# Optimization experiments

Measured on AMD Instinct MI355X. Metric: run time of the kernel, lower is better.

The kernel has to match this reference:

```python
import jax, jax.numpy as jnp
import numpy as np

WS = 7        # window_size
SHIFT = 3     # shift_size
HEADS = 6
DIM = 192
HIDDEN = DIM * 6  # mlp_ratio=6
EPS = 1e-5


def _rel_pos_index(ws):
    # static relative-position index, (ws*ws, ws*ws) int
    coords = np.stack(np.meshgrid(np.arange(ws), np.arange(ws), indexing='ij')).reshape(2, -1)
    rel = coords[:, :, None] - coords[:, None, :]            # (2, N, N)
    rel = rel.transpose(1, 2, 0)                             # (N, N, 2)
    rel[:, :, 0] += ws - 1
    rel[:, :, 1] += ws - 1
    rel[:, :, 0] *= 2 * ws - 1
    return rel.sum(-1)


def _layernorm(t, g, b):
    m = t.mean(-1, keepdims=True)
    v = jnp.mean((t - m) ** 2, axis=-1, keepdims=True)
    return (t - m) * jax.lax.rsqrt(v + EPS) * g + b


def setup_inputs() -> dict:
    key = jax.random.key(0)
    ks = jax.random.split(key, 8)
    B, H, W = 16, 56, 56
    x = jax.random.normal(ks[0], (B, H * W, DIM), dtype=jnp.float32)
    p = lambda k, s: (jax.random.normal(k, s, dtype=jnp.float32) * 0.02)
    return {
        'x': x, 'H': H, 'W': W,
        'ln1_g': jnp.ones((DIM,), jnp.float32), 'ln1_b': jnp.zeros((DIM,), jnp.float32),
        'qkv_w': p(ks[1], (3 * DIM, DIM)), 'qkv_b': jnp.zeros((3 * DIM,), jnp.float32),
        'rpb': p(ks[2], ((2 * WS - 1) ** 2, HEADS)),
        'proj_w': p(ks[3], (DIM, DIM)), 'proj_b': jnp.zeros((DIM,), jnp.float32),
        'ln2_g': jnp.ones((DIM,), jnp.float32), 'ln2_b': jnp.zeros((DIM,), jnp.float32),
        'fc1_w': p(ks[4], (HIDDEN, DIM)), 'fc1_b': jnp.zeros((HIDDEN,), jnp.float32),
        'fc2_w': p(ks[5], (DIM, HIDDEN)), 'fc2_b': jnp.zeros((DIM,), jnp.float32),
    }


def reference(x, H, W, ln1_g, ln1_b, qkv_w, qkv_b, rpb, proj_w, proj_b,
              ln2_g, ln2_b, fc1_w, fc1_b, fc2_w, fc2_b):
    B, L, C = x.shape
    hd = C // HEADS
    shortcut = x
    h = _layernorm(x, ln1_g, ln1_b).reshape(B, H, W, C)
    pad_r = (WS - W % WS) % WS
    pad_b = (WS - H % WS) % WS
    h = jnp.pad(h, ((0, 0), (0, pad_b), (0, pad_r), (0, 0)))
    Hp, Wp = H + pad_b, W + pad_r
    if SHIFT > 0:
        h = jnp.roll(h, (-SHIFT, -SHIFT), axis=(1, 2))
    # window partition -> (nW*B, WS*WS, C)
    h = h.reshape(B, Hp // WS, WS, Wp // WS, WS, C).transpose(0, 1, 3, 2, 4, 5)
    h = h.reshape(-1, WS * WS, C)
    nB, N, _ = h.shape
    qkv = (h @ qkv_w.T + qkv_b).reshape(nB, N, 3, HEADS, hd).transpose(2, 0, 3, 1, 4)
    q, k, v = qkv[0], qkv[1], qkv[2]       # (nB, heads, N, hd)
    scale = hd ** -0.5
    attn = jnp.einsum('bhnd,bhmd->bhnm', q * scale, k)
    idx = _rel_pos_index(WS)
    bias = rpb[idx.reshape(-1)].reshape(N, N, HEADS).transpose(2, 0, 1)  # (heads, N, N)
    attn = jax.nn.softmax(attn + bias[None], axis=-1)
    out = jnp.einsum('bhnm,bhmd->bhnd', attn, v).transpose(0, 2, 1, 3).reshape(nB, N, C)
    out = out @ proj_w.T + proj_b
    # window reverse -> (B, Hp, Wp, C)
    out = out.reshape(B, Hp // WS, Wp // WS, WS, WS, C).transpose(0, 1, 3, 2, 4, 5)
    out = out.reshape(B, Hp, Wp, C)
    if SHIFT > 0:
        out = jnp.roll(out, (SHIFT, SHIFT), axis=(1, 2))
    out = out[:, :H, :W, :].reshape(B, H * W, C)
    x = shortcut + out
    h2 = _layernorm(x, ln2_g, ln2_b)
    h2 = jax.nn.gelu(h2 @ fc1_w.T + fc1_b, approximate=False)
    return x + (h2 @ fc2_w.T + fc2_b)
```

## Files before the change

kernel.cpp:

```cpp
#include <hip/hip_runtime.h>

typedef unsigned short u16;
typedef __bf16 bf16x8 __attribute__((ext_vector_type(8)));
typedef float f32x4 __attribute__((ext_vector_type(4)));

#define AS1 __attribute__((address_space(1)))
#define AS3 __attribute__((address_space(3)))

__device__ __forceinline__ void gld16(const void* g, void* l) {
  __builtin_amdgcn_global_load_lds((const AS1 void*)g, (AS3 void*)l, 16, 0, 0);
}

__device__ __forceinline__ u16 f2bf(float f) {
  union { float f; unsigned int u; } v; v.f = f;
  unsigned int u = v.u;
  u += 0x7fffu + ((u >> 16) & 1u);
  return (u16)(u >> 16);
}
__device__ __forceinline__ float bf2f(u16 h) {
  union { unsigned int u; float f; } v; v.u = ((unsigned int)h) << 16; return v.f;
}
__device__ __forceinline__ float gelu_f(float v) {
  float u = v * (1.5957691216f + 0.0713548163f * v * v);
  return v * __frcp_rn(1.0f + __expf(-u));
}

__global__ __launch_bounds__(256) void cast_weights(
    const float* __restrict__ w0, const float* __restrict__ w1,
    const float* __restrict__ w2, const float* __restrict__ w3,
    u16* __restrict__ o0, u16* __restrict__ o1,
    u16* __restrict__ o2, u16* __restrict__ o3) {
  int i = blockIdx.x * 256 + threadIdx.x;
  if (i < 110592) o0[i] = f2bf(w0[i]);
  if (i < 36864)  o1[i] = f2bf(w1[i]);
  if (i < 221184) o2[i] = f2bf(w2[i]);
  if (i < 221184) o3[i] = f2bf(w3[i]);
}

__global__ __launch_bounds__(256) void build_btab(
    const float* __restrict__ rpb, float* __restrict__ btab) {
  int id = blockIdx.x * 256 + threadIdx.x;
  int head = id >> 12;
  int m = (id >> 6) & 63;
  int r = id & 63;
  float v;
  if (m >= 49) v = -1e30f;
  else if (r >= 49) v = 0.0f;
  else {
    int mi = m / 7, mj = m - mi * 7;
    int ri = r / 7, rj = r - ri * 7;
    v = rpb[((ri - mi + 6) * 13 + (rj - mj + 6)) * 6 + head];
  }
  btab[id] = v;
}

__global__ __launch_bounds__(256) void ln_kernel(
    const float* __restrict__ x, const float* __restrict__ g,
    const float* __restrict__ b, u16* __restrict__ out) {
  int row = blockIdx.x * 4 + (threadIdx.x >> 6);
  int lane = threadIdx.x & 63;
  const float* xr = x + (long)row * 192;
  float e0 = xr[lane], e1 = xr[lane + 64], e2 = xr[lane + 128];
  float s = e0 + e1 + e2;
  #pragma unroll
  for (int o = 1; o < 64; o <<= 1) s += __shfl_xor(s, o);
  float mean = s * (1.0f / 192.0f);
  float d0 = e0 - mean, d1 = e1 - mean, d2 = e2 - mean;
  float q = d0 * d0 + d1 * d1 + d2 * d2;
  #pragma unroll
  for (int o = 1; o < 64; o <<= 1) q += __shfl_xor(q, o);
  float rstd = rsqrtf(q * (1.0f / 192.0f) + 1e-5f);
  u16* orow = out + (long)row * 192;
  orow[lane]       = f2bf(d0 * rstd * g[lane]       + b[lane]);
  orow[lane + 64]  = f2bf(d1 * rstd * g[lane + 64]  + b[lane + 64]);
  orow[lane + 128] = f2bf(d2 * rstd * g[lane + 128] + b[lane + 128]);
}

template<int MODE>
__global__ __launch_bounds__(256, 4) void gemm_kernel(
    const u16* __restrict__ A, const u16* __restrict__ W,
    const float* __restrict__ bias, const float* __restrict__ resid,
    void* __restrict__ out, int N, int K) {
  __shared__ u16 lds[18432];
  float* ct = (float*)lds;
  int tid = threadIdx.x;
  int wave = tid >> 6, lane = tid & 63;
  int wm = wave >> 1, wn = wave & 1;
  int quad = lane >> 4, l15 = lane & 15;
  long bm = (long)blockIdx.x * 128;
  int bn = blockIdx.y * 64;

  f32x4 acc[4][2] = {};
  for (int kc = 0; kc < K; kc += 96) {
    if (kc > 0) __syncthreads();
    int t0 = wave * 9;
    #pragma unroll
    for (int ti = 0; ti < 9; ti++) {
      int t = t0 + ti;
      int isB = t >= 24;
      int tt = isB ? t - 24 : t;
      int grp = tt / 3, kt = tt - grp * 3;
      const u16* g = isB
          ? (W + (long)(bn + grp * 16 + l15) * K + kc + kt * 32 + quad * 8)
          : (A + (bm + grp * 16 + l15) * K + kc + kt * 32 + quad * 8);
      gld16(g, &lds[(isB ? 12288 : 0) + tt * 512]);
    }
    __syncthreads();
    #pragma unroll
    for (int kt = 0; kt < 3; kt++) {
      bf16x8 af[4], bfr[2];
      #pragma unroll
      for (int mt = 0; mt < 4; mt++)
        af[mt] = *(const bf16x8*)&lds[((wm * 4 + mt) * 3 + kt) * 512 + lane * 8];
      #pragma unroll
      for (int nt = 0; nt < 2; nt++)
        bfr[nt] = *(const bf16x8*)&lds[12288 + ((wn * 2 + nt) * 3 + kt) * 512 + lane * 8];
      #pragma unroll
      for (int mt = 0; mt < 4; mt++)
        #pragma unroll
        for (int nt = 0; nt < 2; nt++)
          acc[mt][nt] = __builtin_amdgcn_mfma_f32_16x16x32_bf16(af[mt], bfr[nt], acc[mt][nt], 0, 0, 0);
    }
  }
  __syncthreads();
  #pragma unroll
  for (int nt = 0; nt < 2; nt++) {
    int col = wn * 32 + nt * 16 + l15;
    float bi = bias[bn + col];
    #pragma unroll
    for (int mt = 0; mt < 4; mt++) {
      int row0 = wm * 64 + mt * 16 + quad * 4;
      #pragma unroll
      for (int j = 0; j < 4; j++)
        ct[(row0 + j) * 66 + col] = acc[mt][nt][j] + bi;
    }
  }
  __syncthreads();
  #pragma unroll
  for (int it = 0; it < 8; it++) {
    int c = it * 256 + tid;
    int row = c >> 4, cg = (c & 15) * 4;
    float4 v = *(const float4*)&ct[row * 66 + cg];
    long idx = (bm + row) * (long)N + bn + cg;
    if (MODE == 2) {
      const float4 rv = *(const float4*)(resid + idx);
      v.x += rv.x; v.y += rv.y; v.z += rv.z; v.w += rv.w;
      *(float4*)((float*)out + idx) = v;
    } else {
      if (MODE == 1) {
        v.x = gelu_f(v.x); v.y = gelu_f(v.y); v.z = gelu_f(v.z); v.w = gelu_f(v.w);
      }
      uint2 pk;
      pk.x = (unsigned int)f2bf(v.x) | ((unsigned int)f2bf(v.y) << 16);
      pk.y = (unsigned int)f2bf(v.z) | ((unsigned int)f2bf(v.w) << 16);
      *(uint2*)((u16*)out + idx) = pk;
    }
  }
}

__global__ __launch_bounds__(256) void attn_kernel(
    const u16* __restrict__ qkv, const float* __restrict__ btab,
    u16* __restrict__ attn) {
  __shared__ u16 lds[4 * 7552];
  int tid = threadIdx.x;
  int wave = tid >> 6, lane = tid & 63;
  int quad = lane >> 4, l15 = lane & 15;
  int w = blockIdx.x * 4 + wave;
  int win = w / 6, head = w - win * 6;
  int b = win >> 6, wy = (win >> 3) & 7, wx = win & 7;
  u16* lq = lds + wave * 7552;
  u16* lk = lq + 2560;
  u16* lvt = lq + 5120;
  float* rsum = (float*)(lq + 7424);
  u16* lp = lq;

  #pragma unroll
  for (int p = 0; p < 4; p++) {
    int n = p * 16 + (lane >> 2);
    int qtr = (lane & 3) * 8;
    uint4 qv = {}, kv = {}, vv = {};
    if (n < 49) {
      int i = n / 7, j = n - i * 7;
      int y = wy * 7 + i + 3;  if (y >= 56) y -= 56;
      int xx = wx * 7 + j + 3; if (xx >= 56) xx -= 56;
      long base = ((long)(b * 3136 + y * 56 + xx)) * 576 + head * 32 + qtr;
      qv = *(const uint4*)(qkv + base);
      kv = *(const uint4*)(qkv + base + 192);
      vv = *(const uint4*)(qkv + base + 384);
    }
    *(uint4*)&lq[n * 40 + qtr] = qv;
    *(uint4*)&lk[n * 40 + qtr] = kv;
    const u16* vp = (const u16*)&vv;
    #pragma unroll
    for (int d = 0; d < 8; d++) lvt[(qtr + d) * 72 + n] = vp[d];
  }
  __syncthreads();

  bf16x8 ka[4], qb[4];
  #pragma unroll
  for (int t = 0; t < 4; t++) {
    ka[t] = *(const bf16x8*)&lk[(t * 16 + l15) * 40 + quad * 8];
    qb[t] = *(const bf16x8*)&lq[(t * 16 + l15) * 40 + quad * 8];
  }
  f32x4 s[4][4];
  const f32x4 fz = {0.0f, 0.0f, 0.0f, 0.0f};
  #pragma unroll
  for (int tm = 0; tm < 4; tm++)
    #pragma unroll
    for (int tr = 0; tr < 4; tr++)
      s[tm][tr] = __builtin_amdgcn_mfma_f32_16x16x32_bf16(ka[tm], qb[tr], fz, 0, 0, 0);

  const float scale = 0.17677669529663687f;
  const float* bt = btab + head * 4096;
  float mx[4] = {-1e30f, -1e30f, -1e30f, -1e30f};
  #pragma unroll
  for (int tm = 0; tm < 4; tm++) {
    int m0 = tm * 16 + quad * 4;
    #pragma unroll
    for (int tr = 0; tr < 4; tr++) {
      int r = tr * 16 + l15;
      #pragma unroll
      for (int j = 0; j < 4; j++) {
        float v = s[tm][tr][j] * scale + bt[(m0 + j) * 64 + r];
        s[tm][tr][j] = v;
        mx[tr] = fmaxf(mx[tr], v);
      }
    }
  }
  #pragma unroll
  for (int tr = 0; tr < 4; tr++) {
    mx[tr] = fmaxf(mx[tr], __shfl_xor(mx[tr], 16));
    mx[tr] = fmaxf(mx[tr], __shfl_xor(mx[tr], 32));
  }
  float sm[4] = {0.f, 0.f, 0.f, 0.f};
  #pragma unroll
  for (int tm = 0; tm < 4; tm++) {
    #pragma unroll
    for (int tr = 0; tr < 4; tr++) {
      int r = tr * 16 + l15;
      float e0 = __expf(s[tm][tr][0] - mx[tr]);
      float e1 = __expf(s[tm][tr][1] - mx[tr]);
      float e2 = __expf(s[tm][tr][2] - mx[tr]);
      float e3 = __expf(s[tm][tr][3] - mx[tr]);
      sm[tr] += (e0 + e1) + (e2 + e3);
      uint2 pk;
      pk.x = (unsigned int)f2bf(e0) | ((unsigned int)f2bf(e1) << 16);
      pk.y = (unsigned int)f2bf(e2) | ((unsigned int)f2bf(e3) << 16);
      *(uint2*)&lp[r * 72 + tm * 16 + quad * 4] = pk;
    }
  }
  #pragma unroll
  for (int tr = 0; tr < 4; tr++) {
    sm[tr] += __shfl_xor(sm[tr], 16);
    sm[tr] += __shfl_xor(sm[tr], 32);
  }
  if (quad == 0) {
    #pragma unroll
    for (int tr = 0; tr < 4; tr++) rsum[tr * 16 + l15] = 1.0f / sm[tr];
  }
  __syncthreads();

  f32x4 o[4][2] = {};
  #pragma unroll
  for (int ks = 0; ks < 2; ks++) {
    bf16x8 vb0 = *(const bf16x8*)&lvt[(l15) * 72 + ks * 32 + quad * 8];
    bf16x8 vb1 = *(const bf16x8*)&lvt[(16 + l15) * 72 + ks * 32 + quad * 8];
    #pragma unroll
    for (int rt = 0; rt < 4; rt++) {
      bf16x8 pf = *(const bf16x8*)&lp[(rt * 16 + l15) * 72 + ks * 32 + quad * 8];
      o[rt][0] = __builtin_amdgcn_mfma_f32_16x16x32_bf16(pf, vb0, o[rt][0], 0, 0, 0);
      o[rt][1] = __builtin_amdgcn_mfma_f32_16x16x32_bf16(pf, vb1, o[rt][1], 0, 0, 0);
    }
  }
  #pragma unroll
  for (int rt = 0; rt < 4; rt++) {
    #pragma unroll
    for (int j = 0; j < 4; j++) {
      int r = rt * 16 + quad * 4 + j;
      if (r < 49) {
        float inv = rsum[r];
        int i = r / 7, jj = r - i * 7;
        int y = wy * 7 + i + 3;   if (y >= 56) y -= 56;
        int xx = wx * 7 + jj + 3; if (xx >= 56) xx -= 56;
        long base = ((long)(b * 3136 + y * 56 + xx)) * 192 + head * 32 + l15;
        attn[base]      = f2bf(o[rt][0][j] * inv);
        attn[base + 16] = f2bf(o[rt][1][j] * inv);
      }
    }
  }
}

extern "C" void kernel_launch(void* const* d_in, const int* in_sizes, int n_in,
                              void* d_out, int out_size, void* d_ws, size_t ws_size,
                              hipStream_t stream) {
  (void)in_sizes; (void)n_in; (void)out_size; (void)ws_size;
  const float* x      = (const float*)d_in[0];
  const float* ln1_g  = (const float*)d_in[3];
  const float* ln1_b  = (const float*)d_in[4];
  const float* qkv_w  = (const float*)d_in[5];
  const float* qkv_b  = (const float*)d_in[6];
  const float* rpb    = (const float*)d_in[7];
  const float* proj_w = (const float*)d_in[8];
  const float* proj_b = (const float*)d_in[9];
  const float* ln2_g  = (const float*)d_in[10];
  const float* ln2_b  = (const float*)d_in[11];
  const float* fc1_w  = (const float*)d_in[12];
  const float* fc1_b  = (const float*)d_in[13];
  const float* fc2_w  = (const float*)d_in[14];
  const float* fc2_b  = (const float*)d_in[15];

  char* ws = (char*)d_ws;
  float* x2   = (float*)(ws + 0);
  u16* hA     = (u16*)(ws + 38535168);
  float* btab = (float*)(ws + 38535168);
  u16* qkv    = (u16*)(ws + 57802752);
  u16* attn   = (u16*)(ws + 115605504);
  u16* hid    = (u16*)(ws + 57802752);
  u16* wbuf   = (u16*)(ws + 173408256);
  u16* qkv_wb  = wbuf;
  u16* proj_wb = wbuf + 110592;
  u16* fc1_wb  = wbuf + 147456;
  u16* fc2_wb  = wbuf + 368640;

  cast_weights<<<dim3(864), 256, 0, stream>>>(qkv_w, proj_w, fc1_w, fc2_w,
                                              qkv_wb, proj_wb, fc1_wb, fc2_wb);
  ln_kernel<<<dim3(12544), 256, 0, stream>>>(x, ln1_g, ln1_b, hA);
  gemm_kernel<0><<<dim3(392, 9), 256, 0, stream>>>(hA, qkv_wb, qkv_b, nullptr,
                                                   qkv, 576, 192);
  build_btab<<<dim3(96), 256, 0, stream>>>(rpb, btab);
  attn_kernel<<<dim3(1536), 256, 0, stream>>>(qkv, btab, attn);
  gemm_kernel<2><<<dim3(392, 3), 256, 0, stream>>>(attn, proj_wb, proj_b, x,
                                                   x2, 192, 192);
  ln_kernel<<<dim3(12544), 256, 0, stream>>>(x2, ln2_g, ln2_b, hA);
  gemm_kernel<1><<<dim3(392, 18), 256, 0, stream>>>(hA, fc1_wb, fc1_b, nullptr,
                                                    hid, 1152, 192);
  gemm_kernel<2><<<dim3(392, 3), 256, 0, stream>>>(hid, fc2_wb, fc2_b, x2,
                                                   (float*)d_out, 192, 1152);
}
```

Measured before the change: 380.9 us.

## Widen GEMM N-tile to 96, load attention Q/K directly to registers, pack bf16 stores

The GEMM block tile grows from 128x64 to 128x96 (three N fragments per wave) with a larger LDS buffer and launch bound lowered to 3, which reduces grid size and reloads of the A tile. The attention kernel now loads Q and K fragments straight from global memory into MFMA registers, dropping their LDS staging and two block barriers. The output is written as packed bf16 pairs, which relies on permuting the proj weight columns in cast_weights. Float-to-bf16 packing and reciprocals use hardware builtins. Risks are lower occupancy and a barrier removal that must stay correct for per-wave LDS use.

Result: faster. 352.9 us (-7.3%).

```diff
diff --git a/kernel.cpp b/kernel.cpp
--- a/kernel.cpp
+++ b/kernel.cpp
@@ -2,6 +2,7 @@
 
 typedef unsigned short u16;
 typedef __bf16 bf16x8 __attribute__((ext_vector_type(8)));
+typedef __bf16 bf16x2_t __attribute__((ext_vector_type(2)));
 typedef float f32x4 __attribute__((ext_vector_type(4)));
 
 #define AS1 __attribute__((address_space(1)))
@@ -20,9 +21,18 @@
 __device__ __forceinline__ float bf2f(u16 h) {
   union { unsigned int u; float f; } v; v.u = ((unsigned int)h) << 16; return v.f;
 }
+__device__ __forceinline__ unsigned int pk2(float a, float b) {
+#if __has_builtin(__builtin_amdgcn_cvt_pk_bf16_f32)
+  union { bf16x2_t v; unsigned int u; } c;
+  c.v = __builtin_amdgcn_cvt_pk_bf16_f32(a, b);
+  return c.u;
+#else
+  return (unsigned int)f2bf(a) | ((unsigned int)f2bf(b) << 16);
+#endif
+}
 __device__ __forceinline__ float gelu_f(float v) {
   float u = v * (1.5957691216f + 0.0713548163f * v * v);
-  return v * __frcp_rn(1.0f + __expf(-u));
+  return v * __builtin_amdgcn_rcpf(1.0f + __expf(-u));
 }
 
 __global__ __launch_bounds__(256) void cast_weights(
@@ -32,7 +42,12 @@
     u16* __restrict__ o2, u16* __restrict__ o3) {
   int i = blockIdx.x * 256 + threadIdx.x;
   if (i < 110592) o0[i] = f2bf(w0[i]);
-  if (i < 36864)  o1[i] = f2bf(w1[i]);
+  if (i < 36864) {
+    int n = i / 192, kp = i - n * 192;
+    int h = kp >> 5, dp = kp & 31;
+    int d = (dp & 1) ? ((dp >> 1) + 16) : (dp >> 1);
+    o1[i] = f2bf(w1[n * 192 + h * 32 + d]);
+  }
   if (i < 221184) o2[i] = f2bf(w2[i]);
   if (i < 221184) o3[i] = f2bf(w3[i]);
 }
@@ -77,26 +92,23 @@
 }
 
 template<int MODE>
-__global__ __launch_bounds__(256, 4) void gemm_kernel(
+__global__ __launch_bounds__(256, 3) void gemm_kernel(
     const u16* __restrict__ A, const u16* __restrict__ W,
     const float* __restrict__ bias, const float* __restrict__ resid,
     void* __restrict__ out, int N, int K) {
-  __shared__ u16 lds[18432];
+  __shared__ u16 lds[25600];
   float* ct = (float*)lds;
-  int tid = threadIdx.x;
-  int wave = tid >> 6, lane = tid & 63;
-  int wm = wave >> 1, wn = wave & 1;
-  int quad = lane >> 4, l15 = lane & 15;
-  long bm = (long)blockIdx.x * 128;
-  int bn = blockIdx.y * 64;
-
-  f32x4 acc[4][2] = {};
+  const int tid = threadIdx.x;
+  const int wave = tid >> 6, lane = tid & 63;
+  const int wm = wave >> 1, wn = wave & 1;
+  const int quad = lane >> 4, l15 = lane & 15;
+  const long bm = (long)blockIdx.x * 128;
+  const int bn = blockIdx.y * 96;
+
+  f32x4 acc[4][3] = {};
   for (int kc = 0; kc < K; kc += 96) {
-    if (kc > 0) __syncthreads();
-    int t0 = wave * 9;
-    #pragma unroll
-    for (int ti = 0; ti < 9; ti++) {
-      int t = t0 + ti;
+    if (kc) __syncthreads();
+    for (int t = wave; t < 42; t += 4) {
       int isB = t >= 24;
       int tt = isB ? t - 24 : t;
       int grp = tt / 3, kt = tt - grp * 3;
@@ -108,40 +120,40 @@
     __syncthreads();
     #pragma unroll
     for (int kt = 0; kt < 3; kt++) {
-      bf16x8 af[4], bfr[2];
+      bf16x8 af[4], bfr[3];
       #pragma unroll
       for (int mt = 0; mt < 4; mt++)
         af[mt] = *(const bf16x8*)&lds[((wm * 4 + mt) * 3 + kt) * 512 + lane * 8];
       #pragma unroll
-      for (int nt = 0; nt < 2; nt++)
-        bfr[nt] = *(const bf16x8*)&lds[12288 + ((wn * 2 + nt) * 3 + kt) * 512 + lane * 8];
+      for (int nt = 0; nt < 3; nt++)
+        bfr[nt] = *(const bf16x8*)&lds[12288 + ((wn * 3 + nt) * 3 + kt) * 512 + lane * 8];
       #pragma unroll
       for (int mt = 0; mt < 4; mt++)
         #pragma unroll
-        for (int nt = 0; nt < 2; nt++)
+        for (int nt = 0; nt < 3; nt++)
           acc[mt][nt] = __builtin_amdgcn_mfma_f32_16x16x32_bf16(af[mt], bfr[nt], acc[mt][nt], 0, 0, 0);
     }
   }
   __syncthreads();
   #pragma unroll
-  for (int nt = 0; nt < 2; nt++) {
-    int col = wn * 32 + nt * 16 + l15;
+  for (int nt = 0; nt < 3; nt++) {
+    int col = wn * 48 + nt * 16 + l15;
     float bi = bias[bn + col];
     #pragma unroll
     for (int mt = 0; mt < 4; mt++) {
       int row0 = wm * 64 + mt * 16 + quad * 4;
       #pragma unroll
       for (int j = 0; j < 4; j++)
-        ct[(row0 + j) * 66 + col] = acc[mt][nt][j] + bi;
+        ct[(row0 + j) * 100 + col] = acc[mt][nt][j] + bi;
     }
   }
   __syncthreads();
   #pragma unroll
-  for (int it = 0; it < 8; it++) {
+  for (int it = 0; it < 12; it++) {
     int c = it * 256 + tid;
-    int row = c >> 4, cg = (c & 15) * 4;
-    float4 v = *(const float4*)&ct[row * 66 + cg];
-    long idx = (bm + row) * (long)N + bn + cg;
+    int row = c / 24, i = c - row * 24;
+    float4 v = *(const float4*)&ct[row * 100 + i * 4];
+    long idx = (bm + row) * (long)N + bn + i * 4;
     if (MODE == 2) {
       const float4 rv = *(const float4*)(resid + idx);
       v.x += rv.x; v.y += rv.y; v.z += rv.z; v.w += rv.w;
@@ -151,8 +163,8 @@
         v.x = gelu_f(v.x); v.y = gelu_f(v.y); v.z = gelu_f(v.z); v.w = gelu_f(v.w);
       }
       uint2 pk;
-      pk.x = (unsigned int)f2bf(v.x) | ((unsigned int)f2bf(v.y) << 16);
-      pk.y = (unsigned int)f2bf(v.z) | ((unsigned int)f2bf(v.w) << 16);
+      pk.x = pk2(v.x, v.y);
+      pk.y = pk2(v.z, v.w);
       *(uint2*)((u16*)out + idx) = pk;
     }
   }
@@ -161,47 +173,38 @@
 __global__ __launch_bounds__(256) void attn_kernel(
     const u16* __restrict__ qkv, const float* __restrict__ btab,
     u16* __restrict__ attn) {
-  __shared__ u16 lds[4 * 7552];
+  __shared__ u16 lds[4 * 7040];
   int tid = threadIdx.x;
   int wave = tid >> 6, lane = tid & 63;
   int quad = lane >> 4, l15 = lane & 15;
   int w = blockIdx.x * 4 + wave;
   int win = w / 6, head = w - win * 6;
   int b = win >> 6, wy = (win >> 3) & 7, wx = win & 7;
-  u16* lq = lds + wave * 7552;
-  u16* lk = lq + 2560;
-  u16* lvt = lq + 5120;
-  float* rsum = (float*)(lq + 7424);
-  u16* lp = lq;
-
-  #pragma unroll
-  for (int p = 0; p < 4; p++) {
-    int n = p * 16 + (lane >> 2);
-    int qtr = (lane & 3) * 8;
-    uint4 qv = {}, kv = {}, vv = {};
+  u16* lp = lds + wave * 7040;
+  u16* lvt = lp + 4608;
+  float* rsum = (float*)(lp + 6912);
+
+  bf16x8 qb[4], ka[4];
+  #pragma unroll
+  for (int t = 0; t < 4; t++) {
+    int n = t * 16 + l15;
+    uint4 qv = {0, 0, 0, 0}, kv = {0, 0, 0, 0}, vv = {0, 0, 0, 0};
     if (n < 49) {
       int i = n / 7, j = n - i * 7;
       int y = wy * 7 + i + 3;  if (y >= 56) y -= 56;
       int xx = wx * 7 + j + 3; if (xx >= 56) xx -= 56;
-      long base = ((long)(b * 3136 + y * 56 + xx)) * 576 + head * 32 + qtr;
+      long base = ((long)(b * 3136 + y * 56 + xx)) * 576 + head * 32 + quad * 8;
       qv = *(const uint4*)(qkv + base);
       kv = *(const uint4*)(qkv + base + 192);
       vv = *(const uint4*)(qkv + base + 384);
     }
-    *(uint4*)&lq[n * 40 + qtr] = qv;
-    *(uint4*)&lk[n * 40 + qtr] = kv;
+    qb[t] = *(const bf16x8*)&qv;
+    ka[t] = *(const bf16x8*)&kv;
     const u16* vp = (const u16*)&vv;
     #pragma unroll
-    for (int d = 0; d < 8; d++) lvt[(qtr + d) * 72 + n] = vp[d];
-  }
-  __syncthreads();
-
-  bf16x8 ka[4], qb[4];
-  #pragma unroll
-  for (int t = 0; t < 4; t++) {
-    ka[t] = *(const bf16x8*)&lk[(t * 16 + l15) * 40 + quad * 8];
-    qb[t] = *(const bf16x8*)&lq[(t * 16 + l15) * 40 + quad * 8];
-  }
+    for (int d = 0; d < 8; d++) lvt[(quad * 8 + d) * 72 + n] = vp[d];
+  }
+
   f32x4 s[4][4];
   const f32x4 fz = {0.0f, 0.0f, 0.0f, 0.0f};
   #pragma unroll
@@ -244,8 +247,8 @@
       float e3 = __expf(s[tm][tr][3] - mx[tr]);
       sm[tr] += (e0 + e1) + (e2 + e3);
       uint2 pk;
-      pk.x = (unsigned int)f2bf(e0) | ((unsigned int)f2bf(e1) << 16);
-      pk.y = (unsigned int)f2bf(e2) | ((unsigned int)f2bf(e3) << 16);
+      pk.x = pk2(e0, e1);
+      pk.y = pk2(e2, e3);
       *(uint2*)&lp[r * 72 + tm * 16 + quad * 4] = pk;
     }
   }
@@ -256,9 +259,8 @@
   }
   if (quad == 0) {
     #pragma unroll
-    for (int tr = 0; tr < 4; tr++) rsum[tr * 16 + l15] = 1.0f / sm[tr];
-  }
-  __syncthreads();
+    for (int tr = 0; tr < 4; tr++) rsum[tr * 16 + l15] = __builtin_amdgcn_rcpf(sm[tr]);
+  }
 
   f32x4 o[4][2] = {};
   #pragma unroll
@@ -282,9 +284,8 @@
         int i = r / 7, jj = r - i * 7;
         int y = wy * 7 + i + 3;   if (y >= 56) y -= 56;
         int xx = wx * 7 + jj + 3; if (xx >= 56) xx -= 56;
-        long base = ((long)(b * 3136 + y * 56 + xx)) * 192 + head * 32 + l15;
-        attn[base]      = f2bf(o[rt][0][j] * inv);
-        attn[base + 16] = f2bf(o[rt][1][j] * inv);
+        long base = ((long)(b * 3136 + y * 56 + xx)) * 192 + head * 32 + 2 * l15;
+        *(unsigned int*)&attn[base] = pk2(o[rt][0][j] * inv, o[rt][1][j] * inv);
       }
     }
   }
@@ -325,15 +326,15 @@
   cast_weights<<<dim3(864), 256, 0, stream>>>(qkv_w, proj_w, fc1_w, fc2_w,
                                               qkv_wb, proj_wb, fc1_wb, fc2_wb);
   ln_kernel<<<dim3(12544), 256, 0, stream>>>(x, ln1_g, ln1_b, hA);
-  gemm_kernel<0><<<dim3(392, 9), 256, 0, stream>>>(hA, qkv_wb, qkv_b, nullptr,
+  gemm_kernel<0><<<dim3(392, 6), 256, 0, stream>>>(hA, qkv_wb, qkv_b, nullptr,
                                                    qkv, 576, 192);
   build_btab<<<dim3(96), 256, 0, stream>>>(rpb, btab);
   attn_kernel<<<dim3(1536), 256, 0, stream>>>(qkv, btab, attn);
-  gemm_kernel<2><<<dim3(392, 3), 256, 0, stream>>>(attn, proj_wb, proj_b, x,
+  gemm_kernel<2><<<dim3(392, 2), 256, 0, stream>>>(attn, proj_wb, proj_b, x,
                                                    x2, 192, 192);
   ln_kernel<<<dim3(12544), 256, 0, stream>>>(x2, ln2_g, ln2_b, hA);
-  gemm_kernel<1><<<dim3(392, 18), 256, 0, stream>>>(hA, fc1_wb, fc1_b, nullptr,
+  gemm_kernel<1><<<dim3(392, 12), 256, 0, stream>>>(hA, fc1_wb, fc1_b, nullptr,
                                                     hid, 1152, 192);
-  gemm_kernel<2><<<dim3(392, 3), 256, 0, stream>>>(hid, fc2_wb, fc2_b, x2,
+  gemm_kernel<2><<<dim3(392, 2), 256, 0, stream>>>(hid, fc2_wb, fc2_b, x2,
                                                    (float*)d_out, 192, 1152);
 }
```
